# Performance work log

Hardware: AMD Instinct MI355X
Metric: run time of the kernel (lower is better)

The kernel has to match this reference:

```python
import jax, jax.numpy as jnp
import numpy as np

NUM_JOINTS = 21

def setup_inputs() -> dict:
    key = jax.random.key(0)
    k1, k2 = jax.random.split(key)
    B = 1048576
    pred = jax.random.normal(k1, (B, NUM_JOINTS * 3), dtype=jnp.float32)
    target = jax.random.normal(k2, (B, NUM_JOINTS * 3), dtype=jnp.float32)
    return {"pred": pred, "target": target}

def reference(pred, target):
    B = pred.shape[0]
    # [B, 21, 3] per-joint coordinates
    p = pred.reshape(B, NUM_JOINTS, 3)
    t = target.reshape(B, NUM_JOINTS, 3)
    # per-joint Euclidean distance, then mean over joints and batch
    d = jnp.sqrt(jnp.sum((p - t) ** 2, axis=-1))  # [B, 21]
    return jnp.mean(d)
```

## Files before the change

### kernel.cpp

```cpp
#include <hip/hip_runtime.h>


#define TPB 256
#define BLOCKS 2048

typedef float f32x4 __attribute__((ext_vector_type(4)));

__global__ __launch_bounds__(TPB) void joint_dist_kernel(
    const float* __restrict__ pred,
    const float* __restrict__ target,
    float* __restrict__ out,
    int ngroups,
    float inv_count)
{
    const f32x4* __restrict__ p4 = (const f32x4*)pred;
    const f32x4* __restrict__ t4 = (const f32x4*)target;

    int tid    = blockIdx.x * TPB + threadIdx.x;
    int stride = gridDim.x * TPB;

    float acc = 0.0f;
    for (int i = tid; i < ngroups; i += stride) {
        int base = i * 3;
        f32x4 a0 = __builtin_nontemporal_load(&p4[base + 0]);
        f32x4 a1 = __builtin_nontemporal_load(&p4[base + 1]);
        f32x4 a2 = __builtin_nontemporal_load(&p4[base + 2]);
        f32x4 b0 = __builtin_nontemporal_load(&t4[base + 0]);
        f32x4 b1 = __builtin_nontemporal_load(&t4[base + 1]);
        f32x4 b2 = __builtin_nontemporal_load(&t4[base + 2]);

        float dx, dy, dz;
        dx = a0.x - b0.x; dy = a0.y - b0.y; dz = a0.z - b0.z;
        acc += sqrtf(dx * dx + dy * dy + dz * dz);
        dx = a0.w - b0.w; dy = a1.x - b1.x; dz = a1.y - b1.y;
        acc += sqrtf(dx * dx + dy * dy + dz * dz);
        dx = a1.z - b1.z; dy = a1.w - b1.w; dz = a2.x - b2.x;
        acc += sqrtf(dx * dx + dy * dy + dz * dz);
        dx = a2.y - b2.y; dy = a2.z - b2.z; dz = a2.w - b2.w;
        acc += sqrtf(dx * dx + dy * dy + dz * dz);
    }

    #pragma unroll
    for (int off = 32; off > 0; off >>= 1)
        acc += __shfl_down(acc, off, 64);

    __shared__ float wsum[TPB / 64];
    int lane = threadIdx.x & 63;
    int wid  = threadIdx.x >> 6;
    if (lane == 0) wsum[wid] = acc;
    __syncthreads();

    if (threadIdx.x == 0) {
        float bsum = wsum[0] + wsum[1] + wsum[2] + wsum[3];
        atomicAdd(out, bsum * inv_count);
    }
}

extern "C" void kernel_launch(void* const* d_in, const int* in_sizes, int n_in,
                              void* d_out, int out_size, void* d_ws, size_t ws_size,
                              hipStream_t stream) {
    const float* pred   = (const float*)d_in[0];
    const float* target = (const float*)d_in[1];
    float* out = (float*)d_out;

    int total_floats = in_sizes[0];
    int ngroups      = total_floats / 12;
    int njoints      = total_floats / 3;

    joint_dist_kernel<<<BLOCKS, TPB, 0, stream>>>(pred, target, out, ngroups,
                                                  1.0f / (float)njoints);
}
```

Baseline: 492.5 us.

## Coalesce loads per wave and regroup xyz triples via ds_bpermute

Each wave now reads a contiguous 3 KB chunk with fully coalesced 16-byte loads, where before each thread read its own strided 48-byte block. The squared differences are then redistributed across lanes with 36 ds_bpermute operations per iteration so every lane can rebuild four xyz triples. The aim is better memory coalescing in a bandwidth-bound kernel, paid for with a lot of LDS-crossbar permute traffic and selects. The chunk count also drops any tail that is not a multiple of 768 floats.

```diff
diff --git a/kernel.cpp b/kernel.cpp
--- a/kernel.cpp
+++ b/kernel.cpp
@@ -10,34 +10,65 @@
     const float* __restrict__ pred,
     const float* __restrict__ target,
     float* __restrict__ out,
-    int ngroups,
+    int nchunks,
     float inv_count)
 {
     const f32x4* __restrict__ p4 = (const f32x4*)pred;
     const f32x4* __restrict__ t4 = (const f32x4*)target;
 
-    int tid    = blockIdx.x * TPB + threadIdx.x;
-    int stride = gridDim.x * TPB;
+    const int lane   = threadIdx.x & 63;
+    const int wave   = (blockIdx.x * TPB + threadIdx.x) >> 6;
+    const int nwaves = (gridDim.x * TPB) >> 6;
+
+    int addr0, addr1, addr2;
+    int r0, r1, r2;
+    {
+        int u0 = 3 * lane + 0, u1 = 3 * lane + 1, u2 = 3 * lane + 2;
+        addr0 = (u0 & 63) << 2; r0 = u0 >> 6;
+        addr1 = (u1 & 63) << 2; r1 = u1 >> 6;
+        addr2 = (u2 & 63) << 2; r2 = u2 >> 6;
+    }
 
     float acc = 0.0f;
-    for (int i = tid; i < ngroups; i += stride) {
-        int base = i * 3;
-        f32x4 a0 = __builtin_nontemporal_load(&p4[base + 0]);
-        f32x4 a1 = __builtin_nontemporal_load(&p4[base + 1]);
-        f32x4 a2 = __builtin_nontemporal_load(&p4[base + 2]);
-        f32x4 b0 = __builtin_nontemporal_load(&t4[base + 0]);
-        f32x4 b1 = __builtin_nontemporal_load(&t4[base + 1]);
-        f32x4 b2 = __builtin_nontemporal_load(&t4[base + 2]);
+    for (int c = wave; c < nchunks; c += nwaves) {
+        const int base = c * 192 + lane;
+        f32x4 pa0 = __builtin_nontemporal_load(&p4[base]);
+        f32x4 pa1 = __builtin_nontemporal_load(&p4[base + 64]);
+        f32x4 pa2 = __builtin_nontemporal_load(&p4[base + 128]);
+        f32x4 tb0 = __builtin_nontemporal_load(&t4[base]);
+        f32x4 tb1 = __builtin_nontemporal_load(&t4[base + 64]);
+        f32x4 tb2 = __builtin_nontemporal_load(&t4[base + 128]);
 
-        float dx, dy, dz;
-        dx = a0.x - b0.x; dy = a0.y - b0.y; dz = a0.z - b0.z;
-        acc += sqrtf(dx * dx + dy * dy + dz * dz);
-        dx = a0.w - b0.w; dy = a1.x - b1.x; dz = a1.y - b1.y;
-        acc += sqrtf(dx * dx + dy * dy + dz * dz);
-        dx = a1.z - b1.z; dy = a1.w - b1.w; dz = a2.x - b2.x;
-        acc += sqrtf(dx * dx + dy * dy + dz * dz);
-        dx = a2.y - b2.y; dy = a2.z - b2.z; dz = a2.w - b2.w;
-        acc += sqrtf(dx * dx + dy * dy + dz * dz);
+        f32x4 d0 = pa0 - tb0, d1 = pa1 - tb1, d2 = pa2 - tb2;
+        f32x4 s0 = d0 * d0,   s1 = d1 * d1,   s2 = d2 * d2;
+
+        float o[12];
+        #pragma unroll
+        for (int k = 0; k < 4; ++k) {
+            {
+                int x0 = __builtin_amdgcn_ds_bpermute(addr0, __float_as_int(s0[k]));
+                int x1 = __builtin_amdgcn_ds_bpermute(addr0, __float_as_int(s1[k]));
+                int x2 = __builtin_amdgcn_ds_bpermute(addr0, __float_as_int(s2[k]));
+                o[0 * 4 + k] = __int_as_float(r0 == 0 ? x0 : (r0 == 1 ? x1 : x2));
+            }
+            {
+                int x0 = __builtin_amdgcn_ds_bpermute(addr1, __float_as_int(s0[k]));
+                int x1 = __builtin_amdgcn_ds_bpermute(addr1, __float_as_int(s1[k]));
+                int x2 = __builtin_amdgcn_ds_bpermute(addr1, __float_as_int(s2[k]));
+                o[1 * 4 + k] = __int_as_float(r1 == 0 ? x0 : (r1 == 1 ? x1 : x2));
+            }
+            {
+                int x0 = __builtin_amdgcn_ds_bpermute(addr2, __float_as_int(s0[k]));
+                int x1 = __builtin_amdgcn_ds_bpermute(addr2, __float_as_int(s1[k]));
+                int x2 = __builtin_amdgcn_ds_bpermute(addr2, __float_as_int(s2[k]));
+                o[2 * 4 + k] = __int_as_float(r2 == 0 ? x0 : (r2 == 1 ? x1 : x2));
+            }
+        }
+
+        acc += sqrtf(o[0] + o[1]  + o[2]);
+        acc += sqrtf(o[3] + o[4]  + o[5]);
+        acc += sqrtf(o[6] + o[7]  + o[8]);
+        acc += sqrtf(o[9] + o[10] + o[11]);
     }
 
     #pragma unroll
@@ -45,8 +76,7 @@
         acc += __shfl_down(acc, off, 64);
 
     __shared__ float wsum[TPB / 64];
-    int lane = threadIdx.x & 63;
-    int wid  = threadIdx.x >> 6;
+    int wid = threadIdx.x >> 6;
     if (lane == 0) wsum[wid] = acc;
     __syncthreads();
 
@@ -64,9 +94,9 @@
     float* out = (float*)d_out;
 
     int total_floats = in_sizes[0];
-    int ngroups      = total_floats / 12;
+    int nchunks      = total_floats / 768;
     int njoints      = total_floats / 3;
 
-    joint_dist_kernel<<<BLOCKS, TPB, 0, stream>>>(pred, target, out, ngroups,
+    joint_dist_kernel<<<BLOCKS, TPB, 0, stream>>>(pred, target, out, nchunks,
                                                   1.0f / (float)njoints);
 }
```

After: 467.7 us. 5.0% less time.
